# Performance work log

Hardware: AMD Instinct MI355X
Metric: run time of the kernel (lower is better)

Reference implementation:

```python
import jax, jax.numpy as jnp
import numpy as np

N_NODES = 4096
N_EDGES = 131072
IN_DIM = 40
HID = 128
OUT = 128
GAT_H = 2
GAT_C = 64
D_MODEL = 128
N_HEAD = 4
FF_DIM = 2048
N_LAYERS = 2
EPS = 1e-5
NEG_SLOPE = 0.2


def _layer_norm(x, g, b):
    mu = x.mean(-1, keepdims=True)
    var = ((x - mu) ** 2).mean(-1, keepdims=True)
    return (x - mu) / jnp.sqrt(var + EPS) * g + b


def _gat_conv(h, src, dst, W, a_src, a_dst, bias):
    # PyG GATConv, concat=True, eval mode (no dropout). Self loops already in (src, dst).
    N = h.shape[0]
    xw = (h @ W.T).reshape(N, GAT_H, GAT_C)          # [N, H, C]
    al_src = (xw * a_src).sum(-1)                     # [N, H]
    al_dst = (xw * a_dst).sum(-1)                     # [N, H]
    e = jax.nn.leaky_relu(al_src[src] + al_dst[dst], NEG_SLOPE)  # [E, H]
    # segment softmax over incoming edges of each dst node
    m = jax.ops.segment_max(e, dst, num_segments=N)
    ex = jnp.exp(e - m[dst])
    s = jax.ops.segment_sum(ex, dst, num_segments=N)
    alpha = ex / (s[dst] + 1e-16)                     # [E, H]
    out = jax.ops.segment_sum(xw[src] * alpha[..., None], dst, num_segments=N)
    return out.reshape(N, GAT_H * GAT_C) + bias


def _encoder_layer(x, p):
    # post-norm nn.TransformerEncoderLayer, relu FFN, eval mode
    (in_w, in_b, out_w, out_b, ln1_g, ln1_b,
     ff_w1, ff_b1, ff_w2, ff_b2, ln2_g, ln2_b) = p
    S, E = x.shape
    Dh = E // N_HEAD
    qkv = x @ in_w.T + in_b                           # [S, 3E]
    q, k, v = [t.reshape(S, N_HEAD, Dh) for t in jnp.split(qkv, 3, axis=-1)]
    scores = jnp.einsum('shd,thd->hst', q, k) / jnp.asarray(np.sqrt(Dh), x.dtype)
    attn = jax.nn.softmax(scores, axis=-1)            # [H, S, S]
    o = jnp.einsum('hst,thd->shd', attn, v).reshape(S, E) @ out_w.T + out_b
    x = _layer_norm(x + o, ln1_g, ln1_b)
    ff = jax.nn.relu(x @ ff_w1.T + ff_b1) @ ff_w2.T + ff_b2
    return _layer_norm(x + ff, ln2_g, ln2_b)


def _forward(floats, edge_index):
    (x, enc_w1, enc_b1, enc_w2, enc_b2,
     gat_w, gat_asrc, gat_adst, gat_b,
     l0_in_w, l0_in_b, l0_out_w, l0_out_b, l0_ln1_g, l0_ln1_b,
     l0_ff_w1, l0_ff_b1, l0_ff_w2, l0_ff_b2, l0_ln2_g, l0_ln2_b,
     l1_in_w, l1_in_b, l1_out_w, l1_out_b, l1_ln1_g, l1_ln1_b,
     l1_ff_w1, l1_ff_b1, l1_ff_w2, l1_ff_b2, l1_ln2_g, l1_ln2_b) = floats
    N = x.shape[0]
    # encoder MLP
    h = jax.nn.relu(x @ enc_w1.T + enc_b1) @ enc_w2.T + enc_b2
    # add one self loop per node (GATConv add_self_loops semantics)
    loop = jnp.arange(N, dtype=edge_index.dtype)
    src = jnp.concatenate([edge_index[0], loop])
    dst = jnp.concatenate([edge_index[1], loop])
    h = _gat_conv(h, src, dst, gat_w, gat_asrc, gat_adst, gat_b)
    layers = [
        (l0_in_w, l0_in_b, l0_out_w, l0_out_b, l0_ln1_g, l0_ln1_b,
         l0_ff_w1, l0_ff_b1, l0_ff_w2, l0_ff_b2, l0_ln2_g, l0_ln2_b),
        (l1_in_w, l1_in_b, l1_out_w, l1_out_b, l1_ln1_g, l1_ln1_b,
         l1_ff_w1, l1_ff_b1, l1_ff_w2, l1_ff_b2, l1_ln2_g, l1_ln2_b),
    ]
    for p in layers:
        h = _encoder_layer(h, p)
    return h


def setup_inputs() -> dict:
    key = jax.random.key(0)
    ks = jax.random.split(key, 40)
    s = 0.05
    inp = {}
    inp['x'] = jax.random.normal(ks[0], (N_NODES, IN_DIM), dtype=jnp.float32)
    # edges with src != dst (self loops added inside reference)
    src = jax.random.randint(ks[1], (N_EDGES,), 0, N_NODES)
    off = jax.random.randint(ks[2], (N_EDGES,), 1, N_NODES)
    dst = (src + off) % N_NODES
    inp['edge_index'] = jnp.stack([src, dst]).astype(jnp.int64)
    inp['enc_w1'] = jax.random.normal(ks[3], (HID, IN_DIM)) * s
    inp['enc_b1'] = jnp.zeros((HID,), jnp.float32)
    inp['enc_w2'] = jax.random.normal(ks[4], (OUT, HID)) * s
    inp['enc_b2'] = jnp.zeros((OUT,), jnp.float32)
    inp['gat_w'] = jax.random.normal(ks[5], (GAT_H * GAT_C, OUT)) * s
    inp['gat_asrc'] = jax.random.normal(ks[6], (GAT_H, GAT_C)) * s
    inp['gat_adst'] = jax.random.normal(ks[7], (GAT_H, GAT_C)) * s
    inp['gat_b'] = jnp.zeros((GAT_H * GAT_C,), jnp.float32)
    for i in range(N_LAYERS):
        k = jax.random.split(ks[8 + i], 8)
        inp[f'l{i}_in_w'] = jax.random.normal(k[0], (3 * D_MODEL, D_MODEL)) * s
        inp[f'l{i}_in_b'] = jnp.zeros((3 * D_MODEL,), jnp.float32)
        inp[f'l{i}_out_w'] = jax.random.normal(k[1], (D_MODEL, D_MODEL)) * s
        inp[f'l{i}_out_b'] = jnp.zeros((D_MODEL,), jnp.float32)
        inp[f'l{i}_ln1_g'] = jnp.ones((D_MODEL,), jnp.float32)
        inp[f'l{i}_ln1_b'] = jnp.zeros((D_MODEL,), jnp.float32)
        inp[f'l{i}_ff_w1'] = jax.random.normal(k[2], (FF_DIM, D_MODEL)) * s
        inp[f'l{i}_ff_b1'] = jnp.zeros((FF_DIM,), jnp.float32)
        inp[f'l{i}_ff_w2'] = jax.random.normal(k[3], (D_MODEL, FF_DIM)) * s
        inp[f'l{i}_ff_b2'] = jnp.zeros((D_MODEL,), jnp.float32)
        inp[f'l{i}_ln2_g'] = jnp.ones((D_MODEL,), jnp.float32)
        inp[f'l{i}_ln2_b'] = jnp.zeros((D_MODEL,), jnp.float32)
    return inp


def reference(x, edge_index, enc_w1, enc_b1, enc_w2, enc_b2,
              gat_w, gat_asrc, gat_adst, gat_b,
              l0_in_w, l0_in_b, l0_out_w, l0_out_b, l0_ln1_g, l0_ln1_b,
              l0_ff_w1, l0_ff_b1, l0_ff_w2, l0_ff_b2, l0_ln2_g, l0_ln2_b,
              l1_in_w, l1_in_b, l1_out_w, l1_out_b, l1_ln1_g, l1_ln1_b,
              l1_ff_w1, l1_ff_b1, l1_ff_w2, l1_ff_b2, l1_ln2_g, l1_ln2_b):
    floats = (x, enc_w1, enc_b1, enc_w2, enc_b2,
              gat_w, gat_asrc, gat_adst, gat_b,
              l0_in_w, l0_in_b, l0_out_w, l0_out_b, l0_ln1_g, l0_ln1_b,
              l0_ff_w1, l0_ff_b1, l0_ff_w2, l0_ff_b2, l0_ln2_g, l0_ln2_b,
              l1_in_w, l1_in_b, l1_out_w, l1_out_b, l1_ln1_g, l1_ln1_b,
              l1_ff_w1, l1_ff_b1, l1_ff_w2, l1_ff_b2, l1_ln2_g, l1_ln2_b)
    return _forward(floats, edge_index)
```

## Files before the change

kernel.cpp:

```cpp
#include <hip/hip_runtime.h>
#include <hip/hip_bf16.h>

typedef __hip_bfloat16 bf16;

#define N_NODES 4096
#define IN_DIM  40
#define DM      128
#define FF_DIM  2048
#define GAT_H   2
#define GAT_C   64
#define NHEAD   4
#define DH      32
#define LN_EPS  1e-5f
#define KSPLIT  4
#define FSPLIT  4

typedef short s8v __attribute__((ext_vector_type(8)));
typedef float f4v __attribute__((ext_vector_type(4)));

#define WO_ENC1 0
#define WO_ENC2 8192
#define WO_GAT  24576
#define WO_L(L) (40960 + (L) * 589824)
#define WO_IN(L)  (WO_L(L))
#define WO_OUT(L) (WO_L(L) + 49152)
#define WO_FF1(L) (WO_L(L) + 65536)
#define WO_FF2(L) (WO_L(L) + 327680)
#define WBUF_ELEMS 1220608

__device__ __forceinline__ float anyload(const void* p, size_t i, int isbf) {
    if (isbf) return __bfloat162float(((const bf16*)p)[i]);
    return ((const float*)p)[i];
}
__device__ __forceinline__ int geti(const int* ei, int i, int is64) {
    return is64 ? ei[2 * (size_t)i] : ei[i];
}
__device__ __forceinline__ ushort tob(float v) {
    bf16 b = __float2bfloat16(v);
    return *(ushort*)&b;
}

__global__ __launch_bounds__(256) void setup_kernel(const void* ones_vec, const int* ei,
                                                    int* flags, int* __restrict__ deg,
                                                    const void* enc_w1, const void* enc_w2,
                                                    const void* gat_w,
                                                    const void* in_w0, const void* out_w0,
                                                    const void* ff_w10, const void* ff_w20,
                                                    const void* in_w1, const void* out_w1,
                                                    const void* ff_w11, const void* ff_w21,
                                                    ushort* __restrict__ wbuf) {
    const int isbf = (((const unsigned*)ones_vec)[0] == 0x3F803F80u) ? 1 : 0;
    int gid = blockIdx.x * 256 + threadIdx.x;
    if (gid < N_NODES) deg[gid] = 0;
    if (gid == 0) {
        flags[0] = isbf;
        const unsigned* e = (const unsigned*)ei;
        flags[1] = (e[1] == 0u && e[3] == 0u && e[5] == 0u && e[7] == 0u) ? 1 : 0;
    }
    int base = gid * 4;
#pragma unroll
    for (int j = 0; j < 4; ++j) {
        int i = base + j;
        if (i >= WBUF_ELEMS) break;
        if (i < WO_ENC2) {
            int r = i >> 6, c = i & 63;
            float v = (c < IN_DIM) ? anyload(enc_w1, (size_t)r * IN_DIM + c, isbf) : 0.f;
            wbuf[i] = tob(v);
            continue;
        }
        const void* s;
        int si;
        if      (i < WO_GAT)     { s = enc_w2; si = i - WO_ENC2; }
        else if (i < WO_L(0))    { s = gat_w;  si = i - WO_GAT; }
        else if (i < WO_OUT(0))  { s = in_w0;  si = i - WO_IN(0); }
        else if (i < WO_FF1(0))  { s = out_w0; si = i - WO_OUT(0); }
        else if (i < WO_FF2(0))  { s = ff_w10; si = i - WO_FF1(0); }
        else if (i < WO_L(1))    { s = ff_w20; si = i - WO_FF2(0); }
        else if (i < WO_OUT(1))  { s = in_w1;  si = i - WO_IN(1); }
        else if (i < WO_FF1(1))  { s = out_w1; si = i - WO_OUT(1); }
        else if (i < WO_FF2(1))  { s = ff_w11; si = i - WO_FF1(1); }
        else                     { s = ff_w21; si = i - WO_FF2(1); }
        wbuf[i] = isbf ? ((const ushort*)s)[si] : tob(((const float*)s)[si]);
    }
}

#define K128STR 136

__global__ __launch_bounds__(256) void encgat_kernel(const void* __restrict__ X,
                                                     const void* __restrict__ b1v,
                                                     const void* __restrict__ b2v,
                                                     const ushort* __restrict__ wbuf,
                                                     const void* __restrict__ asrc,
                                                     const void* __restrict__ adst,
                                                     float* __restrict__ xwout,
                                                     float* __restrict__ als,
                                                     float* __restrict__ ald,
                                                     const int* __restrict__ flags) {
    const int isbf = flags[0];
    const int t = threadIdx.x;
    const int w = t >> 6, lane = t & 63;
    const int col = lane & 15, quad = lane >> 4;
    const int row0 = blockIdx.x * 16;
    __shared__ __align__(16) ushort As[16 * K128STR];
    __shared__ __align__(16) ushort Ws[128 * K128STR];
    __shared__ float Cs[16][132];

    {
        int r = t >> 4, c0 = (t & 15) * 4;
#pragma unroll
        for (int j = 0; j < 4; ++j) {
            int c = c0 + j;
            float v = (c < IN_DIM) ? anyload(X, (size_t)(row0 + r) * IN_DIM + c, isbf) : 0.f;
            As[r * K128STR + c] = tob(v);
        }
    }
#pragma unroll
    for (int i = 0; i < 4; ++i) {
        int idx = t + i * 256;
        int r = idx >> 3, c = (idx & 7) * 8;
        *(uint4*)&Ws[r * 72 + c] = *(const uint4*)&wbuf[WO_ENC1 + r * 64 + c];
    }
    __syncthreads();
    f4v zero = {0.f, 0.f, 0.f, 0.f};
    f4v acc1[2] = {zero, zero};
    {
        s8v a0 = *(const s8v*)&As[col * K128STR + quad * 8];
        s8v a1 = *(const s8v*)&As[col * K128STR + 32 + quad * 8];
#pragma unroll
        for (int nc = 0; nc < 2; ++nc) {
            s8v b0 = *(const s8v*)&Ws[(w * 32 + nc * 16 + col) * 72 + quad * 8];
            s8v b1 = *(const s8v*)&Ws[(w * 32 + nc * 16 + col) * 72 + 32 + quad * 8];
            acc1[nc] = __builtin_amdgcn_mfma_f32_16x16x32_bf16(a0, b0, acc1[nc], 0, 0, 0);
            acc1[nc] = __builtin_amdgcn_mfma_f32_16x16x32_bf16(a1, b1, acc1[nc], 0, 0, 0);
        }
    }
    __syncthreads();
#pragma unroll
    for (int nc = 0; nc < 2; ++nc) {
        int cc = w * 32 + nc * 16 + col;
        float bv = anyload(b1v, cc, isbf);
#pragma unroll
        for (int r = 0; r < 4; ++r)
            As[(quad * 4 + r) * K128STR + cc] = tob(fmaxf(acc1[nc][r] + bv, 0.f));
    }
#pragma unroll
    for (int i = 0; i < 8; ++i) {
        int idx = t + i * 256;
        int r = idx >> 4, c = (idx & 15) * 8;
        *(uint4*)&Ws[r * K128STR + c] = *(const uint4*)&wbuf[WO_ENC2 + r * DM + c];
    }
    __syncthreads();
    f4v acc2[2] = {zero, zero};
#pragma unroll
    for (int j = 0; j < 4; ++j) {
        s8v a = *(const s8v*)&As[col * K128STR + j * 32 + quad * 8];
#pragma unroll
        for (int nc = 0; nc < 2; ++nc) {
            s8v b = *(const s8v*)&Ws[(w * 32 + nc * 16 + col) * K128STR + j * 32 + quad * 8];
            acc2[nc] = __builtin_amdgcn_mfma_f32_16x16x32_bf16(a, b, acc2[nc], 0, 0, 0);
        }
    }
    __syncthreads();
#pragma unroll
    for (int nc = 0; nc < 2; ++nc) {
        int cc = w * 32 + nc * 16 + col;
        float bv = anyload(b2v, cc, isbf);
#pragma unroll
        for (int r = 0; r < 4; ++r)
            As[(quad * 4 + r) * K128STR + cc] = tob(acc2[nc][r] + bv);
    }
#pragma unroll
    for (int i = 0; i < 8; ++i) {
        int idx = t + i * 256;
        int r = idx >> 4, c = (idx & 15) * 8;
        *(uint4*)&Ws[r * K128STR + c] = *(const uint4*)&wbuf[WO_GAT + r * DM + c];
    }
    __syncthreads();
    f4v acc3[2] = {zero, zero};
#pragma unroll
    for (int j = 0; j < 4; ++j) {
        s8v a = *(const s8v*)&As[col * K128STR + j * 32 + quad * 8];
#pragma unroll
        for (int nc = 0; nc < 2; ++nc) {
            s8v b = *(const s8v*)&Ws[(w * 32 + nc * 16 + col) * K128STR + j * 32 + quad * 8];
            acc3[nc] = __builtin_amdgcn_mfma_f32_16x16x32_bf16(a, b, acc3[nc], 0, 0, 0);
        }
    }
#pragma unroll
    for (int nc = 0; nc < 2; ++nc) {
        int cc = w * 32 + nc * 16 + col;
#pragma unroll
        for (int r = 0; r < 4; ++r) {
            int row = quad * 4 + r;
            float v = acc3[nc][r];
            xwout[(size_t)(row0 + row) * DM + cc] = v;
            Cs[row][cc] = v;
        }
    }
    __syncthreads();
#pragma unroll
    for (int rr = 0; rr < 4; ++rr) {
        int row = w * 4 + rr;
        float x0 = Cs[row][lane], x1 = Cs[row][64 + lane];
        float s0 = x0 * anyload(asrc, lane, isbf);
        float d0 = x0 * anyload(adst, lane, isbf);
        float s1 = x1 * anyload(asrc, 64 + lane, isbf);
        float d1 = x1 * anyload(adst, 64 + lane, isbf);
#pragma unroll
        for (int o = 32; o >= 1; o >>= 1) {
            s0 += __shfl_xor(s0, o); d0 += __shfl_xor(d0, o);
            s1 += __shfl_xor(s1, o); d1 += __shfl_xor(d1, o);
        }
        if (lane == 0) {
            int n = row0 + row;
            als[n * 2 + 0] = s0; ald[n * 2 + 0] = d0;
            als[n * 2 + 1] = s1; ald[n * 2 + 1] = d1;
        }
    }
}

__global__ __launch_bounds__(256) void gemm32_kernel(const ushort* __restrict__ A,
                                                     const ushort* __restrict__ Wb,
                                                     const void* __restrict__ bias,
                                                     ushort* __restrict__ Cb,
                                                     ushort* __restrict__ vtb,
                                                     int N,
                                                     const int* __restrict__ flags,
                                                     int relu) {
    const int isbf = flags[0];
    const int t = threadIdx.x;
    const int w = t >> 6, lane = t & 63;
    const int col = lane & 15, quad = lane >> 4;
    const int wr = (w & 1) * 16, wc = (w >> 1) * 32;
    const int row0 = blockIdx.y * 32, col0 = blockIdx.x * 64;
    __shared__ __align__(16) ushort As[32 * K128STR];
    __shared__ __align__(16) ushort Ws[64 * K128STR];
#pragma unroll
    for (int i = 0; i < 2; ++i) {
        int idx = t + i * 256;
        int r = idx >> 4, c = (idx & 15) * 8;
        *(uint4*)&As[r * K128STR + c] = *(const uint4*)&A[(size_t)(row0 + r) * DM + c];
    }
#pragma unroll
    for (int i = 0; i < 4; ++i) {
        int idx = t + i * 256;
        int r = idx >> 4, c = (idx & 15) * 8;
        *(uint4*)&Ws[r * K128STR + c] = *(const uint4*)&Wb[(size_t)(col0 + r) * DM + c];
    }
    __syncthreads();
    f4v zero = {0.f, 0.f, 0.f, 0.f};
    f4v acc[2] = {zero, zero};
#pragma unroll
    for (int j = 0; j < 4; ++j) {
        s8v a = *(const s8v*)&As[(wr + col) * K128STR + j * 32 + quad * 8];
#pragma unroll
        for (int nc = 0; nc < 2; ++nc) {
            s8v b = *(const s8v*)&Ws[(wc + nc * 16 + col) * K128STR + j * 32 + quad * 8];
            acc[nc] = __builtin_amdgcn_mfma_f32_16x16x32_bf16(a, b, acc[nc], 0, 0, 0);
        }
    }
#pragma unroll
    for (int nc = 0; nc < 2; ++nc) {
        int cc = col0 + wc + nc * 16 + col;
        float bv = bias ? anyload(bias, cc, isbf) : 0.f;
#pragma unroll
        for (int r = 0; r < 4; ++r) {
            int rr = row0 + wr + quad * 4 + r;
            float v = acc[nc][r] + bv;
            if (relu) v = fmaxf(v, 0.f);
            Cb[(size_t)rr * N + cc] = tob(v);
            if (vtb && cc >= 256) vtb[(size_t)(cc - 256) * N_NODES + rr] = tob(v);
        }
    }
}

__global__ __launch_bounds__(256) void oproj_ln_kernel(const float* __restrict__ pO,
                                                       const float* __restrict__ pL,
                                                       const ushort* __restrict__ Wb,
                                                       const void* __restrict__ bias,
                                                       float* __restrict__ h,
                                                       ushort* __restrict__ hb,
                                                       const void* __restrict__ g,
                                                       const void* __restrict__ b,
                                                       const int* __restrict__ flags) {
    const int isbf = flags[0];
    const int t = threadIdx.x;
    const int w = t >> 6, lane = t & 63;
    const int col = lane & 15, quad = lane >> 4;
    const int row0 = blockIdx.x * 16;
    __shared__ __align__(16) ushort As[16 * K128STR];
    __shared__ __align__(16) ushort Ws[128 * K128STR];
    __shared__ float Cs[16][132];

    {
        int ar = t >> 4, ac = (t & 15) * 8;
        int rr = row0 + ar;
        int hh = ac >> 5, d0 = ac & 31;
        size_t qi0 = ((size_t)rr) * NHEAD + hh;
        float lsum = 0.f;
        float osum[8] = {};
#pragma unroll
        for (int kz = 0; kz < KSPLIT; ++kz) {
            size_t qi = qi0 + (size_t)kz * N_NODES * NHEAD;
            lsum += pL[qi];
            const float* po = &pO[qi * 32 + d0];
#pragma unroll
            for (int j = 0; j < 8; ++j) osum[j] += po[j];
        }
        float inv = 1.f / lsum;
#pragma unroll
        for (int j = 0; j < 8; ++j) As[ar * K128STR + ac + j] = tob(osum[j] * inv);
    }
#pragma unroll
    for (int i = 0; i < 8; ++i) {
        int idx = t + i * 256;
        int r = idx >> 4, c = (idx & 15) * 8;
        *(uint4*)&Ws[r * K128STR + c] = *(const uint4*)&Wb[(size_t)r * DM + c];
    }
    __syncthreads();
    f4v zero = {0.f, 0.f, 0.f, 0.f};
    f4v acc[2] = {zero, zero};
#pragma unroll
    for (int j = 0; j < 4; ++j) {
        s8v a = *(const s8v*)&As[col * K128STR + j * 32 + quad * 8];
#pragma unroll
        for (int nc = 0; nc < 2; ++nc) {
            s8v b = *(const s8v*)&Ws[(w * 32 + nc * 16 + col) * K128STR + j * 32 + quad * 8];
            acc[nc] = __builtin_amdgcn_mfma_f32_16x16x32_bf16(a, b, acc[nc], 0, 0, 0);
        }
    }
#pragma unroll
    for (int nc = 0; nc < 2; ++nc) {
        int cc = w * 32 + nc * 16 + col;
        float bv = bias ? anyload(bias, cc, isbf) : 0.f;
#pragma unroll
        for (int r = 0; r < 4; ++r)
            Cs[quad * 4 + r][cc] = acc[nc][r] + bv;
    }
    __syncthreads();
#pragma unroll
    for (int rr = 0; rr < 4; ++rr) {
        int row = w * 4 + rr;
        size_t base = (size_t)(row0 + row) * DM;
        float v0 = h[base + lane] + Cs[row][lane];
        float v1 = h[base + 64 + lane] + Cs[row][64 + lane];
        float s = v0 + v1;
#pragma unroll
        for (int o = 32; o >= 1; o >>= 1) s += __shfl_xor(s, o);
        float mu = s * (1.f / DM);
        float d0 = v0 - mu, d1 = v1 - mu;
        float q = d0 * d0 + d1 * d1;
#pragma unroll
        for (int o = 32; o >= 1; o >>= 1) q += __shfl_xor(q, o);
        float rstd = rsqrtf(q * (1.f / DM) + LN_EPS);
        float o0 = d0 * rstd * anyload(g, lane, isbf) + anyload(b, lane, isbf);
        float o1 = d1 * rstd * anyload(g, 64 + lane, isbf) + anyload(b, 64 + lane, isbf);
        h[base + lane] = o0;       h[base + 64 + lane] = o1;
        hb[base + lane] = tob(o0); hb[base + 64 + lane] = tob(o1);
    }
}

__global__ __launch_bounds__(256) void ff2_splitk_kernel(const ushort* __restrict__ A,
                                                         const ushort* __restrict__ Wb,
                                                         float* __restrict__ Cpart) {
    const int t = threadIdx.x;
    const int w = t >> 6, lane = t & 63;
    const int col = lane & 15, quad = lane >> 4;
    const int row0 = blockIdx.x * 64;
    const int ks = blockIdx.y;
    const int k_beg = ks * (FF_DIM / FSPLIT);
    __shared__ __align__(16) ushort As[64 * K128STR];
    __shared__ __align__(16) ushort Ws[128 * K128STR];
    f4v zero = {0.f, 0.f, 0.f, 0.f};
    f4v acc[8] = {zero, zero, zero, zero, zero, zero, zero, zero};
    const int wr = w * 16;

    for (int it = 0; it < 4; ++it) {
        int k0 = k_beg + it * 128;
        __syncthreads();
#pragma unroll
        for (int i = 0; i < 4; ++i) {
            int idx = t + i * 256;
            int r = idx >> 4, c = (idx & 15) * 8;
            *(uint4*)&As[r * K128STR + c] = *(const uint4*)&A[(size_t)(row0 + r) * FF_DIM + k0 + c];
        }
#pragma unroll
        for (int i = 0; i < 8; ++i) {
            int idx = t + i * 256;
            int r = idx >> 4, c = (idx & 15) * 8;
            *(uint4*)&Ws[r * K128STR + c] = *(const uint4*)&Wb[(size_t)r * FF_DIM + k0 + c];
        }
        __syncthreads();
#pragma unroll
        for (int j = 0; j < 4; ++j) {
            s8v a = *(const s8v*)&As[(wr + col) * K128STR + j * 32 + quad * 8];
#pragma unroll
            for (int nc = 0; nc < 8; ++nc) {
                s8v b = *(const s8v*)&Ws[(nc * 16 + col) * K128STR + j * 32 + quad * 8];
                acc[nc] = __builtin_amdgcn_mfma_f32_16x16x32_bf16(a, b, acc[nc], 0, 0, 0);
            }
        }
    }
#pragma unroll
    for (int nc = 0; nc < 8; ++nc) {
        int cc = nc * 16 + col;
#pragma unroll
        for (int r = 0; r < 4; ++r) {
            int rr = row0 + wr + quad * 4 + r;
            Cpart[((size_t)ks * N_NODES + rr) * DM + cc] = acc[nc][r];
        }
    }
}

__global__ __launch_bounds__(256) void ln4_kernel(float* __restrict__ h,
                                                  const float* __restrict__ pC,
                                                  const void* __restrict__ fbias,
                                                  ushort* __restrict__ hb,
                                                  const void* __restrict__ g, const void* __restrict__ b,
                                                  void* __restrict__ outp,
                                                  const int* __restrict__ flags) {
    const int isbf = flags[0];
    const int row = blockIdx.x * 4 + (threadIdx.x >> 6);
    const int lane = threadIdx.x & 63;
    const size_t base = (size_t)row * DM;
    float y0 = anyload(fbias, lane, isbf), y1 = anyload(fbias, 64 + lane, isbf);
#pragma unroll
    for (int kz = 0; kz < FSPLIT; ++kz) {
        size_t pb = (size_t)kz * N_NODES * DM + base;
        y0 += pC[pb + lane];
        y1 += pC[pb + 64 + lane];
    }
    float v0 = h[base + lane] + y0;
    float v1 = h[base + 64 + lane] + y1;
    float s = v0 + v1;
#pragma unroll
    for (int o = 32; o >= 1; o >>= 1) s += __shfl_xor(s, o);
    float mu = s * (1.f / DM);
    float d0 = v0 - mu, d1 = v1 - mu;
    float q = d0 * d0 + d1 * d1;
#pragma unroll
    for (int o = 32; o >= 1; o >>= 1) q += __shfl_xor(q, o);
    float rstd = rsqrtf(q * (1.f / DM) + LN_EPS);
    float o0 = d0 * rstd * anyload(g, lane, isbf) + anyload(b, lane, isbf);
    float o1 = d1 * rstd * anyload(g, 64 + lane, isbf) + anyload(b, 64 + lane, isbf);
    h[base + lane] = o0;       h[base + 64 + lane] = o1;
    hb[base + lane] = tob(o0); hb[base + 64 + lane] = tob(o1);
    if (outp) {
        if (isbf) {
            ((ushort*)outp)[base + lane] = tob(o0);
            ((ushort*)outp)[base + 64 + lane] = tob(o1);
        } else {
            ((float*)outp)[base + lane] = o0;
            ((float*)outp)[base + 64 + lane] = o1;
        }
    }
}

__global__ void deg_hist_kernel(const int* __restrict__ ei, int E0,
                                int* __restrict__ deg, const int* __restrict__ flags) {
    const int is64 = flags[1];
    int e = blockIdx.x * 256 + threadIdx.x;
    int E = E0 + N_NODES;
    if (e >= E) return;
    int d = (e < E0) ? geti(ei, E0 + e, is64) : (e - E0);
    atomicAdd(&deg[d], 1);
}

__global__ __launch_bounds__(256) void scan_kernel(const int* __restrict__ deg,
                                                   int* __restrict__ rowptr,
                                                   int* __restrict__ cursor) {
    __shared__ int part[256];
    const int t = threadIdx.x;
    const int base = t * 16;
    int loc[16];
    int s = 0;
#pragma unroll
    for (int i = 0; i < 16; ++i) { loc[i] = s; s += deg[base + i]; }
    part[t] = s;
    __syncthreads();
    for (int d = 1; d < 256; d <<= 1) {
        int v = (t >= d) ? part[t - d] : 0;
        __syncthreads();
        part[t] += v;
        __syncthreads();
    }
    int prev = (t == 0) ? 0 : part[t - 1];
#pragma unroll
    for (int i = 0; i < 16; ++i) {
        int r = prev + loc[i];
        rowptr[base + i] = r;
        cursor[base + i] = r;
    }
    if (t == 255) rowptr[N_NODES] = part[255];
}

__global__ void scatter_kernel(const int* __restrict__ ei, int E0,
                               int* __restrict__ cursor, int* __restrict__ csr_src,
                               const int* __restrict__ flags) {
    const int is64 = flags[1];
    int e = blockIdx.x * 256 + threadIdx.x;
    int E = E0 + N_NODES;
    if (e >= E) return;
    int s = (e < E0) ? geti(ei, e, is64) : (e - E0);
    int d = (e < E0) ? geti(ei, E0 + e, is64) : (e - E0);
    int pos = atomicAdd(&cursor[d], 1);
    csr_src[pos] = s;
}

__global__ __launch_bounds__(256) void gat_gather_kernel(const int* __restrict__ rowptr,
                                                         const int* __restrict__ csr_src,
                                                         const float* __restrict__ als,
                                                         const float* __restrict__ ald,
                                                         const float* __restrict__ xw,
                                                         const void* __restrict__ gat_b,
                                                         float* __restrict__ hg,
                                                         ushort* __restrict__ hgb,
                                                         const int* __restrict__ flags) {
    const int isbf = flags[0];
    const int idx = blockIdx.x * 4 + (threadIdx.x >> 6);
    const int lane = threadIdx.x & 63;
    const int d = idx >> 1, hh = idx & 1;
    const int beg = rowptr[d], end = rowptr[d + 1];
    const float aldv = ald[d * 2 + hh];

    float mx = -3.0e38f;
    for (int i = beg + lane; i < end; i += 64) {
        int s = csr_src[i];
        float v = als[s * 2 + hh] + aldv;
        v = (v > 0.f) ? v : 0.2f * v;
        mx = fmaxf(mx, v);
    }
#pragma unroll
    for (int o = 32; o >= 1; o >>= 1) mx = fmaxf(mx, __shfl_xor(mx, o));
    float sm = 0.f;
    for (int i = beg + lane; i < end; i += 64) {
        int s = csr_src[i];
        float v = als[s * 2 + hh] + aldv;
        v = (v > 0.f) ? v : 0.2f * v;
        sm += __expf(v - mx);
    }
#pragma unroll
    for (int o = 32; o >= 1; o >>= 1) sm += __shfl_xor(sm, o);
    const float inv = 1.f / (sm + 1e-16f);

    float o_acc = 0.f;
    for (int i = beg; i < end; ++i) {
        int s = csr_src[i];
        float v = als[s * 2 + hh] + aldv;
        v = (v > 0.f) ? v : 0.2f * v;
        float alpha = __expf(v - mx) * inv;
        o_acc += alpha * xw[(size_t)s * DM + hh * GAT_C + lane];
    }
    float outv = o_acc + anyload(gat_b, hh * GAT_C + lane, isbf);
    size_t off = (size_t)d * DM + hh * GAT_C + lane;
    hg[off] = outv;
    hgb[off] = tob(outv);
}

#define KSTR 40
#define VSTR 136
#define PSTR 136
__global__ __launch_bounds__(256) void attn_mfma_kernel(const ushort* __restrict__ qkvb,
                                                        const ushort* __restrict__ vtb,
                                                        float* __restrict__ pO,
                                                        float* __restrict__ pL) {
    const int hh = blockIdx.y;
    const int kz = blockIdx.z;
    const int t = threadIdx.x;
    const int w = t >> 6;
    const int lane = t & 63;
    const int col = lane & 15;
    const int quad = lane >> 4;
    const int qr = blockIdx.x * 64 + w * 16;

    __shared__ __align__(16) ushort Ks[128 * KSTR];
    __shared__ __align__(16) ushort Vt[32 * VSTR];
    __shared__ __align__(16) ushort Pl[4][16 * PSTR];

    s8v aq = *(const s8v*)&qkvb[(size_t)(qr + col) * 384 + hh * 32 + quad * 8];

    f4v zero = {0.f, 0.f, 0.f, 0.f};
    f4v of[2] = {zero, zero};
    float lacc[4] = {0.f, 0.f, 0.f, 0.f};
    const float scale = 0.17677669529663687f;
    const int k_beg = kz * (N_NODES / KSPLIT);
    const int k_end = k_beg + (N_NODES / KSPLIT);

    for (int kt = k_beg; kt < k_end; kt += 128) {
        __syncthreads();
        for (int idx = t; idx < 512; idx += 256) {
            int r = idx >> 2, c = (idx & 3) * 8;
            *(uint4*)&Ks[r * KSTR + c] =
                *(const uint4*)&qkvb[(size_t)(kt + r) * 384 + 128 + hh * 32 + c];
        }
        for (int idx = t; idx < 512; idx += 256) {
            int d = idx >> 4, c = (idx & 15) * 8;
            *(uint4*)&Vt[d * VSTR + c] =
                *(const uint4*)&vtb[(size_t)(hh * 32 + d) * N_NODES + kt + c];
        }
        __syncthreads();

        f4v sf[8];
#pragma unroll
        for (int kb = 0; kb < 8; ++kb) {
            s8v bk = *(const s8v*)&Ks[(kb * 16 + col) * KSTR + quad * 8];
            sf[kb] = __builtin_amdgcn_mfma_f32_16x16x32_bf16(aq, bk, zero, 0, 0, 0);
        }
#pragma unroll
        for (int kb = 0; kb < 8; ++kb) {
#pragma unroll
            for (int r = 0; r < 4; ++r) {
                float p = __expf(sf[kb][r] * scale);
                lacc[r] += p;
                Pl[w][(quad * 4 + r) * PSTR + kb * 16 + col] = tob(p);
            }
        }
#pragma unroll
        for (int kc = 0; kc < 4; ++kc) {
            s8v ap = *(const s8v*)&Pl[w][col * PSTR + kc * 32 + quad * 8];
#pragma unroll
            for (int nc = 0; nc < 2; ++nc) {
                s8v bv = *(const s8v*)&Vt[(nc * 16 + col) * VSTR + kc * 32 + quad * 8];
                of[nc] = __builtin_amdgcn_mfma_f32_16x16x32_bf16(ap, bv, of[nc], 0, 0, 0);
            }
        }
    }
#pragma unroll
    for (int r = 0; r < 4; ++r) {
        float lv = lacc[r];
#pragma unroll
        for (int off = 1; off <= 8; off <<= 1) lv += __shfl_xor(lv, off);
        int row = quad * 4 + r;
        size_t qi = ((size_t)kz * N_NODES + qr + row) * NHEAD + hh;
#pragma unroll
        for (int nc = 0; nc < 2; ++nc)
            pO[qi * 32 + nc * 16 + col] = of[nc][r];
        if (col == 0) pL[qi] = lv;
    }
}

extern "C" void kernel_launch(void* const* d_in, const int* in_sizes, int n_in,
                              void* d_out, int out_size, void* d_ws, size_t ws_size,
                              hipStream_t stream) {
    const void* x        = d_in[0];
    const int*  ei       = (const int*)d_in[1];
    const void* enc_w1   = d_in[2];
    const void* enc_b1   = d_in[3];
    const void* enc_w2   = d_in[4];
    const void* enc_b2   = d_in[5];
    const void* gat_w    = d_in[6];
    const void* gat_asrc = d_in[7];
    const void* gat_adst = d_in[8];
    const void* gat_b    = d_in[9];
    const void *in_w[2], *in_b[2], *out_w[2], *out_b[2], *ln1_g[2], *ln1_b[2];
    const void *ff_w1[2], *ff_b1[2], *ff_w2[2], *ff_b2[2], *ln2_g[2], *ln2_b[2];
    for (int L = 0; L < 2; ++L) {
        int base = 10 + L * 12;
        in_w[L]  = d_in[base + 0];
        in_b[L]  = d_in[base + 1];
        out_w[L] = d_in[base + 2];
        out_b[L] = d_in[base + 3];
        ln1_g[L] = d_in[base + 4];
        ln1_b[L] = d_in[base + 5];
        ff_w1[L] = d_in[base + 6];
        ff_b1[L] = d_in[base + 7];
        ff_w2[L] = d_in[base + 8];
        ff_b2[L] = d_in[base + 9];
        ln2_g[L] = d_in[base + 10];
        ln2_b[L] = d_in[base + 11];
    }
    const int E0 = in_sizes[1] / 2;
    const int E  = E0 + N_NODES;
    const size_t NN = N_NODES;

    int*    flags   = (int*)d_ws;
    float*  h       = (float*)d_ws + 64;
    ushort* hb      = (ushort*)(h + NN * DM);
    ushort* qkvb    = hb + NN * DM;
    ushort* vtb     = qkvb + NN * 384;
    ushort* ff1b    = vtb + NN * DM;
    ushort* wbuf    = ff1b + NN * FF_DIM;
    float*  pO      = (float*)(wbuf + WBUF_ELEMS);
    float*  pL      = pO + (size_t)KSPLIT * NN * NHEAD * 32;
    float*  pC      = pL + (size_t)KSPLIT * NN * NHEAD;
    float*  xw      = pC + (size_t)FSPLIT * NN * DM;
    float*  als     = xw + NN * DM;
    float*  ald     = als + NN * GAT_H;
    int*    deg     = (int*)(ald + NN * GAT_H);
    int*    rowptr  = deg + N_NODES;
    int*    cursor  = rowptr + N_NODES + 1;
    int*    csr_src = cursor + N_NODES;

    dim3 blk(256);

    setup_kernel<<<dim3((WBUF_ELEMS + 1023) / 1024), blk, 0, stream>>>(
        ln1_g[0], ei, flags, deg,
        enc_w1, enc_w2, gat_w, in_w[0], out_w[0], ff_w1[0], ff_w2[0],
        in_w[1], out_w[1], ff_w1[1], ff_w2[1], wbuf);
    deg_hist_kernel<<<dim3((E + 255) / 256), blk, 0, stream>>>(ei, E0, deg, flags);
    scan_kernel<<<dim3(1), blk, 0, stream>>>(deg, rowptr, cursor);
    scatter_kernel<<<dim3((E + 255) / 256), blk, 0, stream>>>(ei, E0, cursor, csr_src, flags);

    encgat_kernel<<<dim3(N_NODES / 16), blk, 0, stream>>>(
        x, enc_b1, enc_b2, wbuf, gat_asrc, gat_adst, xw, als, ald, flags);
    gat_gather_kernel<<<dim3(N_NODES * GAT_H / 4), blk, 0, stream>>>(
        rowptr, csr_src, als, ald, xw, gat_b, h, hb, flags);

    for (int L = 0; L < 2; ++L) {
        gemm32_kernel<<<dim3(3 * DM / 64, N_NODES / 32), blk, 0, stream>>>(
            hb, wbuf + WO_IN(L), in_b[L], qkvb, vtb, 3 * DM, flags, 0);
        attn_mfma_kernel<<<dim3(N_NODES / 64, NHEAD, KSPLIT), blk, 0, stream>>>(
            qkvb, vtb, pO, pL);
        oproj_ln_kernel<<<dim3(N_NODES / 16), blk, 0, stream>>>(
            pO, pL, wbuf + WO_OUT(L), out_b[L], h, hb, ln1_g[L], ln1_b[L], flags);
        gemm32_kernel<<<dim3(FF_DIM / 64, N_NODES / 32), blk, 0, stream>>>(
            hb, wbuf + WO_FF1(L), ff_b1[L], ff1b, nullptr, FF_DIM, flags, 1);
        ff2_splitk_kernel<<<dim3(N_NODES / 64, FSPLIT), blk, 0, stream>>>(
            ff1b, wbuf + WO_FF2(L), pC);
        ln4_kernel<<<dim3(N_NODES / 4), blk, 0, stream>>>(
            h, pC, ff_b2[L], hb, ln2_g[L], ln2_b[L],
            (L == 1) ? d_out : nullptr, flags);
    }
}
```

Measured before the change: 318.1 us.

## Fuse FF2 split-K reduction and LayerNorm via last-block atomic counter; raise attention KSPLIT

Result: slower. 368.0 us (+15.7%).

```diff
diff --git a/kernel.cpp b/kernel.cpp
--- a/kernel.cpp
+++ b/kernel.cpp
@@ -12,7 +12,7 @@
 #define NHEAD   4
 #define DH      32
 #define LN_EPS  1e-5f
-#define KSPLIT  4
+#define KSPLIT  8
 #define FSPLIT  4
 
 typedef short s8v __attribute__((ext_vector_type(8)));
@@ -42,6 +42,7 @@
 
 __global__ __launch_bounds__(256) void setup_kernel(const void* ones_vec, const int* ei,
                                                     int* flags, int* __restrict__ deg,
+                                                    int* __restrict__ cnt,
                                                     const void* enc_w1, const void* enc_w2,
                                                     const void* gat_w,
                                                     const void* in_w0, const void* out_w0,
@@ -52,6 +53,7 @@
     const int isbf = (((const unsigned*)ones_vec)[0] == 0x3F803F80u) ? 1 : 0;
     int gid = blockIdx.x * 256 + threadIdx.x;
     if (gid < N_NODES) deg[gid] = 0;
+    if (gid < 128) cnt[gid] = 0;
     if (gid == 0) {
         flags[0] = isbf;
         const unsigned* e = (const unsigned*)ei;
@@ -362,7 +364,16 @@
 
 __global__ __launch_bounds__(256) void ff2_splitk_kernel(const ushort* __restrict__ A,
                                                          const ushort* __restrict__ Wb,
-                                                         float* __restrict__ Cpart) {
+                                                         float* __restrict__ Cpart,
+                                                         const void* __restrict__ fbias,
+                                                         float* __restrict__ h,
+                                                         ushort* __restrict__ hb,
+                                                         const void* __restrict__ g,
+                                                         const void* __restrict__ b,
+                                                         void* __restrict__ outp,
+                                                         int* __restrict__ cnt,
+                                                         const int* __restrict__ flags) {
+    const int isbf = flags[0];
     const int t = threadIdx.x;
     const int w = t >> 6, lane = t & 63;
     const int col = lane & 15, quad = lane >> 4;
@@ -371,6 +382,7 @@
     const int k_beg = ks * (FF_DIM / FSPLIT);
     __shared__ __align__(16) ushort As[64 * K128STR];
     __shared__ __align__(16) ushort Ws[128 * K128STR];
+    __shared__ int last_flag;
     f4v zero = {0.f, 0.f, 0.f, 0.f};
     f4v acc[8] = {zero, zero, zero, zero, zero, zero, zero, zero};
     const int wr = w * 16;
@@ -410,48 +422,51 @@
             Cpart[((size_t)ks * N_NODES + rr) * DM + cc] = acc[nc][r];
         }
     }
-}
-
-__global__ __launch_bounds__(256) void ln4_kernel(float* __restrict__ h,
-                                                  const float* __restrict__ pC,
-                                                  const void* __restrict__ fbias,
-                                                  ushort* __restrict__ hb,
-                                                  const void* __restrict__ g, const void* __restrict__ b,
-                                                  void* __restrict__ outp,
-                                                  const int* __restrict__ flags) {
-    const int isbf = flags[0];
-    const int row = blockIdx.x * 4 + (threadIdx.x >> 6);
-    const int lane = threadIdx.x & 63;
-    const size_t base = (size_t)row * DM;
-    float y0 = anyload(fbias, lane, isbf), y1 = anyload(fbias, 64 + lane, isbf);
-#pragma unroll
-    for (int kz = 0; kz < FSPLIT; ++kz) {
-        size_t pb = (size_t)kz * N_NODES * DM + base;
-        y0 += pC[pb + lane];
-        y1 += pC[pb + 64 + lane];
-    }
-    float v0 = h[base + lane] + y0;
-    float v1 = h[base + 64 + lane] + y1;
-    float s = v0 + v1;
-#pragma unroll
-    for (int o = 32; o >= 1; o >>= 1) s += __shfl_xor(s, o);
-    float mu = s * (1.f / DM);
-    float d0 = v0 - mu, d1 = v1 - mu;
-    float q = d0 * d0 + d1 * d1;
-#pragma unroll
-    for (int o = 32; o >= 1; o >>= 1) q += __shfl_xor(q, o);
-    float rstd = rsqrtf(q * (1.f / DM) + LN_EPS);
-    float o0 = d0 * rstd * anyload(g, lane, isbf) + anyload(b, lane, isbf);
-    float o1 = d1 * rstd * anyload(g, 64 + lane, isbf) + anyload(b, 64 + lane, isbf);
-    h[base + lane] = o0;       h[base + 64 + lane] = o1;
-    hb[base + lane] = tob(o0); hb[base + 64 + lane] = tob(o1);
-    if (outp) {
-        if (isbf) {
-            ((ushort*)outp)[base + lane] = tob(o0);
-            ((ushort*)outp)[base + 64 + lane] = tob(o1);
-        } else {
-            ((float*)outp)[base + lane] = o0;
-            ((float*)outp)[base + 64 + lane] = o1;
+    __syncthreads();
+    if (t == 0) {
+        __threadfence();
+        int old = __hip_atomic_fetch_add(&cnt[blockIdx.x], 1,
+                                         __ATOMIC_ACQ_REL, __HIP_MEMORY_SCOPE_AGENT);
+        last_flag = (old == FSPLIT - 1) ? 1 : 0;
+    }
+    __syncthreads();
+    if (!last_flag) return;
+    if (t == 0) __threadfence();
+    __syncthreads();
+
+    for (int rr4 = 0; rr4 < 16; ++rr4) {
+        int row = row0 + rr4 * 4 + w;
+        size_t base = (size_t)row * DM;
+        float y0 = anyload(fbias, lane, isbf), y1 = anyload(fbias, 64 + lane, isbf);
+#pragma unroll
+        for (int kz = 0; kz < FSPLIT; ++kz) {
+            size_t pb = (size_t)kz * N_NODES * DM + base;
+            y0 += Cpart[pb + lane];
+            y1 += Cpart[pb + 64 + lane];
+        }
+        float v0 = h[base + lane] + y0;
+        float v1 = h[base + 64 + lane] + y1;
+        float s = v0 + v1;
+#pragma unroll
+        for (int o = 32; o >= 1; o >>= 1) s += __shfl_xor(s, o);
+        float mu = s * (1.f / DM);
+        float d0 = v0 - mu, d1 = v1 - mu;
+        float q = d0 * d0 + d1 * d1;
+#pragma unroll
+        for (int o = 32; o >= 1; o >>= 1) q += __shfl_xor(q, o);
+        float rstd = rsqrtf(q * (1.f / DM) + LN_EPS);
+        float o0 = d0 * rstd * anyload(g, lane, isbf) + anyload(b, lane, isbf);
+        float o1 = d1 * rstd * anyload(g, 64 + lane, isbf) + anyload(b, 64 + lane, isbf);
+        h[base + lane] = o0;       h[base + 64 + lane] = o1;
+        hb[base + lane] = tob(o0); hb[base + 64 + lane] = tob(o1);
+        if (outp) {
+            if (isbf) {
+                ((ushort*)outp)[base + lane] = tob(o0);
+                ((ushort*)outp)[base + 64 + lane] = tob(o1);
+            } else {
+                ((float*)outp)[base + lane] = o0;
+                ((float*)outp)[base + 64 + lane] = o1;
+            }
         }
     }
 }
@@ -690,11 +705,12 @@
     int*    rowptr  = deg + N_NODES;
     int*    cursor  = rowptr + N_NODES + 1;
     int*    csr_src = cursor + N_NODES;
+    int*    cnt     = csr_src + E + 64;
 
     dim3 blk(256);
 
     setup_kernel<<<dim3((WBUF_ELEMS + 1023) / 1024), blk, 0, stream>>>(
-        ln1_g[0], ei, flags, deg,
+        ln1_g[0], ei, flags, deg, cnt,
         enc_w1, enc_w2, gat_w, in_w[0], out_w[0], ff_w1[0], ff_w2[0],
         in_w[1], out_w[1], ff_w1[1], ff_w2[1], wbuf);
     deg_hist_kernel<<<dim3((E + 255) / 256), blk, 0, stream>>>(ei, E0, deg, flags);
@@ -716,9 +732,7 @@
         gemm32_kernel<<<dim3(FF_DIM / 64, N_NODES / 32), blk, 0, stream>>>(
             hb, wbuf + WO_FF1(L), ff_b1[L], ff1b, nullptr, FF_DIM, flags, 1);
         ff2_splitk_kernel<<<dim3(N_NODES / 64, FSPLIT), blk, 0, stream>>>(
-            ff1b, wbuf + WO_FF2(L), pC);
-        ln4_kernel<<<dim3(N_NODES / 4), blk, 0, stream>>>(
-            h, pC, ff_b2[L], hb, ln2_g[L], ln2_b[L],
-            (L == 1) ? d_out : nullptr, flags);
-    }
-}
+            ff1b, wbuf + WO_FF2(L), pC, ff_b2[L], h, hb, ln2_g[L], ln2_b[L],
+            (L == 1) ? d_out : nullptr, cnt + L * 64, flags);
+    }
+}
```
